# Kernel optimization log

Hardware: AMD Instinct MI355X
Metric: run time of the kernel (lower is better)

The kernel has to match this reference:

```python
import jax, jax.numpy as jnp
import numpy as np

B, T, D = 512, 128, 768
CD, SD, P = 192, 128, 128
FEAT = CD + SD + 1  # 321
LN_EPS = 1e-5


def setup_inputs() -> dict:
    key = jax.random.key(0)
    ks = jax.random.split(key, 10)
    return {
        'H': jax.random.normal(ks[0], (B, T, D), jnp.float32),
        'tt': jax.random.randint(ks[1], (B, T), 0, 2, jnp.int64),
        'attn': jnp.ones((B, T), jnp.int64),
        'Wc': jax.random.normal(ks[2], (CD, 2 * D), jnp.float32) * 0.02,
        'bc': jax.random.normal(ks[3], (CD,), jnp.float32) * 0.02,
        'Ws': jax.random.normal(ks[4], (SD, 2 * D), jnp.float32) * 0.02,
        'bs': jax.random.normal(ks[5], (SD,), jnp.float32) * 0.02,
        'gate': jnp.array([0.5], jnp.float32),
        'ln_g': jnp.ones((FEAT,), jnp.float32),
        'ln_b': jnp.zeros((FEAT,), jnp.float32),
        'Wcls': jax.random.normal(ks[6], (2, FEAT), jnp.float32) * 0.02,
        'bcls': jax.random.normal(ks[7], (2,), jnp.float32) * 0.02,
        'dirs': jax.random.normal(ks[8], (P, D), jnp.float32),
    }


def reference(H, tt, attn, Wc, bc, Ws, bs, gate, ln_g, ln_b, Wcls, bcls, dirs):
    dt = H.dtype
    cls = H[:, 0]                                   # [B, D]
    mask0 = (tt == 0) & (attn == 1)                 # [B, T]
    mask1 = (tt == 1) & (attn == 1)

    def mmean(mask):
        mf = mask.astype(dt)
        s = jnp.einsum('btd,bt->bd', H, mf)
        cnt = jnp.maximum(mask.sum(1, keepdims=True), 1).astype(dt)
        return s / cnt

    rep = jnp.concatenate([cls, mmean(mask0) - mmean(mask1)], axis=1)  # [B, 2D]
    C = rep @ Wc.T + bc
    S = rep @ Ws.T + bs
    g = jax.nn.sigmoid(gate)                        # [1]
    fused = jnp.concatenate([C * (1 - g), S * g], axis=1)  # [B, CD+SD]

    # batched max-sliced W1: project, push masked tokens to +inf, sort along T
    dirs_n = dirs / jnp.linalg.norm(dirs, axis=1, keepdims=True)
    proj = jnp.einsum('btd,pd->btp', H, dirs_n)     # [B, T, P]
    inf = jnp.asarray(jnp.inf, dt)
    xp = jnp.sort(jnp.where(mask0[:, :, None], proj, inf), axis=1)
    yp = jnp.sort(jnp.where(mask1[:, :, None], proj, inf), axis=1)
    n0 = mask0.sum(1)
    n1 = mask1.sum(1)
    mm = jnp.minimum(n0, n1)                        # [B] ragged truncation length
    valid = (jnp.arange(T)[None, :] < mm[:, None])[:, :, None]  # [B, T, 1]
    xs = jnp.where(valid, xp, 0.0)
    ys = jnp.where(valid, yp, 0.0)
    diff = jnp.abs(xs - ys).sum(1) / jnp.maximum(mm, 1)[:, None].astype(dt)  # [B, P]
    d_ot = diff.max(1, keepdims=True)               # [B, 1]

    feat = jnp.concatenate([fused, d_ot], axis=1)   # [B, 321]
    mu = feat.mean(-1, keepdims=True)
    var = feat.var(-1, keepdims=True)
    normed = (feat - mu) / jnp.sqrt(var + LN_EPS) * ln_g + ln_b
    logits = normed @ Wcls.T + bcls                 # [B, 2]

    ortho = jnp.mean((Wc @ Ws.T) ** 2)
    return logits, ortho
```

## Files before the change

kernel.cpp:

```cpp
#include <hip/hip_runtime.h>
#include <hip/hip_bf16.h>

constexpr int B_ = 512;
constexpr int T_ = 128;
constexpr int D_ = 768;
constexpr int CD_ = 192;
constexpr int SD_ = 128;
constexpr int P_ = 128;
constexpr int FEAT_ = 321;
constexpr float LN_EPS_ = 1e-5f;

constexpr size_t REP_SZ   = (size_t)B_ * 2 * D_;
constexpr size_t DN16_FLT = (size_t)P_ * D_ / 2;

typedef __attribute__((ext_vector_type(8))) short short8;
typedef __attribute__((ext_vector_type(4))) float f32x4;

__device__ __forceinline__ unsigned short f2bf(float x) {
    unsigned u = __float_as_uint(x);
    return (unsigned short)((u + 0x7FFFu + ((u >> 16) & 1u)) >> 16);
}
__device__ __forceinline__ float bf2f(unsigned short h) {
    return __uint_as_float((unsigned)h << 16);
}

__global__ __launch_bounds__(256) void k_dirs(const float* __restrict__ dirs,
                                              unsigned short* __restrict__ dn16) {
    int p = blockIdx.x;
    int tid = threadIdx.x;
    float s = 0.f;
    for (int d = tid; d < D_; d += 256) {
        float v = dirs[(size_t)p * D_ + d];
        s = fmaf(v, v, s);
    }
    __shared__ float red[256];
    red[tid] = s;
    __syncthreads();
    for (int off = 128; off > 0; off >>= 1) {
        if (tid < off) red[tid] += red[tid + off];
        __syncthreads();
    }
    float inv = 1.0f / sqrtf(red[0]);
    for (int d = tid; d < D_; d += 256) {
        dn16[(size_t)p * D_ + d] = f2bf(dirs[(size_t)p * D_ + d] * inv);
    }
}

__global__ __launch_bounds__(256) void k_rep(const float* __restrict__ H,
                                             const int* __restrict__ tt,
                                             const int* __restrict__ attn,
                                             float* __restrict__ rep) {
    int b = blockIdx.x;
    int tid = threadIdx.x;
    __shared__ float m0s[T_], m1s[T_];
    __shared__ int ncnt[2];
    if (tid < 2) ncnt[tid] = 0;
    __syncthreads();
    if (tid < T_) {
        int t = tt[b * T_ + tid];
        int a = attn[b * T_ + tid];
        float m0 = (t == 0 && a == 1) ? 1.f : 0.f;
        float m1 = (t == 1 && a == 1) ? 1.f : 0.f;
        m0s[tid] = m0;
        m1s[tid] = m1;
        if (m0 > 0.f) atomicAdd(&ncnt[0], 1);
        if (m1 > 0.f) atomicAdd(&ncnt[1], 1);
    }
    __syncthreads();
    float inv0 = 1.f / (float)max(ncnt[0], 1);
    float inv1 = 1.f / (float)max(ncnt[1], 1);
    const float* Hb = H + (size_t)b * T_ * D_;
    float* repb = rep + (size_t)b * 2 * D_;
#pragma unroll
    for (int pass = 0; pass < 3; ++pass) {
        int d = pass * 256 + tid;
        float s0 = 0.f, s1 = 0.f;
#pragma unroll 8
        for (int t = 0; t < T_; ++t) {
            float h = Hb[(size_t)t * D_ + d];
            s0 = fmaf(h, m0s[t], s0);
            s1 = fmaf(h, m1s[t], s1);
        }
        repb[d] = Hb[d];
        repb[D_ + d] = s0 * inv0 - s1 * inv1;
    }
}

constexpr int NIT_ = 24;
constexpr int BUF_U16_ = 8192;

__global__ __launch_bounds__(512, 2) void k_projsort(const float* __restrict__ H,
                                                     const int* __restrict__ tt,
                                                     const int* __restrict__ attn,
                                                     const unsigned short* __restrict__ dn16,
                                                     float* __restrict__ d_ot) {
    const int b = blockIdx.x;
    const int tid = threadIdx.x;

    __shared__ __align__(16) unsigned short stage[2 * BUF_U16_];
    __shared__ __align__(16) unsigned short proj16[T_ * 128];
    __shared__ float m0s[T_], m1s[T_];
    __shared__ unsigned char pos_s[T_];
    __shared__ int ncnt[2];
    __shared__ float dred[512];

    unsigned char* xb = (unsigned char*)stage;
    unsigned char* yb = xb + 64 * 128;

    if (tid < 2) ncnt[tid] = 0;
    __syncthreads();
    if (tid < T_) {
        int t = tt[b * T_ + tid];
        int a = attn[b * T_ + tid];
        float m0 = (t == 0 && a == 1) ? 1.f : 0.f;
        float m1 = (t == 1 && a == 1) ? 1.f : 0.f;
        m0s[tid] = m0;
        m1s[tid] = m1;
        if (m0 > 0.f) atomicAdd(&ncnt[0], 1);
        if (m1 > 0.f) atomicAdd(&ncnt[1], 1);
    }
    __syncthreads();
    const int n0 = ncnt[0], n1 = ncnt[1];
    const int ntot = n0 + n1;
    if (tid < T_) {
        float me0 = m0s[tid], me1 = m1s[tid];
        unsigned char pp = 0xFF;
        if (me0 > 0.f || me1 > 0.f) {
            bool g1 = (me1 > 0.f);
            const float* ms = g1 ? m1s : m0s;
            int pos = g1 ? n0 : 0;
            for (int j = 0; j < tid; ++j) pos += (ms[j] > 0.f) ? 1 : 0;
            pp = (unsigned char)pos;
        }
        pos_s[tid] = pp;
    }
    __syncthreads();

    const float* Hb = H + (size_t)b * T_ * D_;
    const int srow = tid >> 2;
    const int scp  = tid & 3;
    const int sclog = scp ^ ((srow >> 1) & 3);
    const float* gA = Hb + (size_t)srow * D_ + sclog * 8;
    const unsigned short* gB = dn16 + (size_t)srow * D_ + sclog * 8;
    const int dOff = srow * 32 + scp * 8;

    const int wv = tid >> 6;
    const int wr = wv >> 2;
    const int wc = wv & 3;
    const int lane = tid & 63;
    const int fr = lane & 15;
    const int kg = lane >> 4;
    const int ck = (kg ^ ((fr >> 1) & 3)) * 8;
    const int baseA = (64 * wr + fr) * 32 + ck;
    const int baseB = 4096 + (32 * wc + fr) * 32 + ck;

    f32x4 acc[4][2];
#pragma unroll
    for (int m = 0; m < 4; ++m)
#pragma unroll
        for (int n = 0; n < 2; ++n) acc[m][n] = (f32x4){0.f, 0.f, 0.f, 0.f};

    float4 a0 = *reinterpret_cast<const float4*>(gA);
    float4 a1 = *reinterpret_cast<const float4*>(gA + 4);
    short8 bv = *reinterpret_cast<const short8*>(gB);

    for (int it = 0; it < NIT_; ++it) {
        const int cur = it & 1;
        unsigned short* sb = stage + cur * BUF_U16_;
        short8 w;
        w[0] = (short)f2bf(a0.x); w[1] = (short)f2bf(a0.y);
        w[2] = (short)f2bf(a0.z); w[3] = (short)f2bf(a0.w);
        w[4] = (short)f2bf(a1.x); w[5] = (short)f2bf(a1.y);
        w[6] = (short)f2bf(a1.z); w[7] = (short)f2bf(a1.w);
        *reinterpret_cast<short8*>(sb + dOff) = w;
        *reinterpret_cast<short8*>(sb + 4096 + dOff) = bv;
        if (it < NIT_ - 1) {
            int k = (it + 1) * 32;
            a0 = *reinterpret_cast<const float4*>(gA + k);
            a1 = *reinterpret_cast<const float4*>(gA + k + 4);
            bv = *reinterpret_cast<const short8*>(gB + k);
        }
        asm volatile("s_waitcnt lgkmcnt(0)" ::: "memory");
        __builtin_amdgcn_s_barrier();
        asm volatile("" ::: "memory");

        const unsigned short* sr = stage + cur * BUF_U16_;
        short8 af[4], bf_[2];
#pragma unroll
        for (int m = 0; m < 4; ++m)
            af[m] = *reinterpret_cast<const short8*>(sr + baseA + 512 * m);
#pragma unroll
        for (int n = 0; n < 2; ++n)
            bf_[n] = *reinterpret_cast<const short8*>(sr + baseB + 512 * n);
#pragma unroll
        for (int m = 0; m < 4; ++m)
#pragma unroll
            for (int n = 0; n < 2; ++n)
                acc[m][n] = __builtin_amdgcn_mfma_f32_16x16x32_bf16(af[m], bf_[n], acc[m][n], 0, 0, 0);

        asm volatile("" ::: "memory");
        __builtin_amdgcn_s_barrier();
        asm volatile("" ::: "memory");
    }

#pragma unroll
    for (int m = 0; m < 4; ++m) {
        int row0 = 64 * wr + 16 * m + kg * 4;
#pragma unroll
        for (int r = 0; r < 4; ++r) {
            int pp = pos_s[row0 + r];
            if (pp != 0xFF) {
#pragma unroll
                for (int n = 0; n < 2; ++n) {
                    int col = 32 * wc + 16 * n + fr;
                    unsigned bb = f2bf(acc[m][n][r]);
                    unsigned su = bb ^ ((bb >> 15) ? 0xFFFFu : 0x8000u);
                    proj16[pp * 128 + col] = (unsigned short)su;
                }
            }
        }
    }
    __syncthreads();

    const int mmv = min(n0, n1);
    const int c = tid & 127;
    const int q = tid >> 7;
#pragma unroll
    for (int pass = 0; pass < 2; ++pass) {
        const int pbase = q * 32 + pass * 16;
        unsigned kv[16];
        int cnt[16];
#pragma unroll
        for (int ii = 0; ii < 16; ++ii) {
            int p = pbase + ii;
            unsigned key = 0xFFFFFFFFu;
            if (p < ntot) {
                unsigned su = proj16[p * 128 + c];
                key = ((unsigned)(p >= n0) << 31) | (su << 8) | (unsigned)p;
            }
            kv[ii] = key;
            cnt[ii] = 0;
        }
        int lo, hi;
        if (pbase + 16 <= n0) { lo = 0;  hi = n0;   }
        else if (pbase >= n0) { lo = n0; hi = ntot; }
        else                  { lo = 0;  hi = ntot; }
        for (int j = lo; j < hi; ++j) {
            unsigned su = proj16[j * 128 + c];
            unsigned kw = ((unsigned)(j >= n0) << 31) | (su << 8) | (unsigned)j;
#pragma unroll
            for (int ii = 0; ii < 16; ++ii) cnt[ii] += (kw < kv[ii]) ? 1 : 0;
        }
#pragma unroll
        for (int ii = 0; ii < 16; ++ii) {
            int p = pbase + ii;
            if (p < ntot) {
                int rank = cnt[ii] - ((p >= n0 && lo == 0) ? n0 : 0);
                if (rank < mmv) {
                    unsigned char* buf = (p >= n0) ? yb : xb;
                    buf[rank * 128 + c] = (unsigned char)p;
                }
            }
        }
    }
    __syncthreads();

    float part = 0.f;
    for (int r = q; r < mmv; r += 4) {
        unsigned sx = proj16[(int)xb[r * 128 + c] * 128 + c];
        unsigned sy = proj16[(int)yb[r * 128 + c] * 128 + c];
        unsigned bx = sx ^ ((sx >> 15) ? 0x8000u : 0xFFFFu);
        unsigned by = sy ^ ((sy >> 15) ? 0x8000u : 0xFFFFu);
        part += fabsf(bf2f((unsigned short)bx) - bf2f((unsigned short)by));
    }
    dred[tid] = part;
    __syncthreads();
    if (tid < 128) {
        float invm = 1.f / (float)max(mmv, 1);
        dred[tid] = (dred[tid] + dred[tid + 128] + dred[tid + 256] + dred[tid + 384]) * invm;
    }
    __syncthreads();
    if (tid < 64) {
        float m = fmaxf(dred[tid], dred[tid + 64]);
#pragma unroll
        for (int off = 32; off > 0; off >>= 1) m = fmaxf(m, __shfl_xor(m, off));
        if (tid == 0) d_ot[b] = m;
    }
}

__global__ __launch_bounds__(320) void k_head(const float* __restrict__ rep,
                                              const float* __restrict__ Wc,
                                              const float* __restrict__ bc,
                                              const float* __restrict__ Ws,
                                              const float* __restrict__ bs,
                                              const float* __restrict__ gate,
                                              const float* __restrict__ lng,
                                              const float* __restrict__ lnb,
                                              const float* __restrict__ Wcls,
                                              const float* __restrict__ bcls,
                                              const float* __restrict__ d_ot,
                                              float* __restrict__ out) {
    int b0 = blockIdx.x * 4;
    int tid = threadIdx.x;
    __shared__ __align__(16) float repS[4 * 1536];
    __shared__ float featS[4 * FEAT_];

    const float4* repg = reinterpret_cast<const float4*>(rep + (size_t)b0 * 1536);
    float4* repl = reinterpret_cast<float4*>(repS);
    for (int i = tid; i < 1536; i += 320) repl[i] = repg[i];
    __syncthreads();

    float g = 1.f / (1.f + expf(-gate[0]));

    {
        int o = tid;
        bool isC = o < CD_;
        const float* w = isC ? (Wc + (size_t)o * 1536) : (Ws + (size_t)(o - CD_) * 1536);
        float bias = isC ? bc[o] : bs[o - CD_];
        float scale = isC ? (1.f - g) : g;
        const float4* w4 = reinterpret_cast<const float4*>(w);
        float a0 = 0.f, a1 = 0.f, a2 = 0.f, a3 = 0.f;
        for (int k4 = 0; k4 < 384; ++k4) {
            float4 wv = w4[k4];
            float4 r0 = repl[k4];
            float4 r1 = repl[384 + k4];
            float4 r2 = repl[768 + k4];
            float4 r3 = repl[1152 + k4];
            a0 += fmaf(wv.x, r0.x, fmaf(wv.y, r0.y, fmaf(wv.z, r0.z, wv.w * r0.w)));
            a1 += fmaf(wv.x, r1.x, fmaf(wv.y, r1.y, fmaf(wv.z, r1.z, wv.w * r1.w)));
            a2 += fmaf(wv.x, r2.x, fmaf(wv.y, r2.y, fmaf(wv.z, r2.z, wv.w * r2.w)));
            a3 += fmaf(wv.x, r3.x, fmaf(wv.y, r3.y, fmaf(wv.z, r3.z, wv.w * r3.w)));
        }
        featS[0 * FEAT_ + o] = (a0 + bias) * scale;
        featS[1 * FEAT_ + o] = (a1 + bias) * scale;
        featS[2 * FEAT_ + o] = (a2 + bias) * scale;
        featS[3 * FEAT_ + o] = (a3 + bias) * scale;
    }
    if (tid < 4) featS[tid * FEAT_ + 320] = d_ot[b0 + tid];
    __syncthreads();

    int w = tid >> 6, lane = tid & 63;
    if (w < 4) {
        const float* f = featS + w * FEAT_;
        float s = 0.f, s2 = 0.f;
        for (int i = lane; i < FEAT_; i += 64) {
            float v = f[i];
            s += v;
            s2 = fmaf(v, v, s2);
        }
#pragma unroll
        for (int off = 32; off > 0; off >>= 1) {
            s += __shfl_xor(s, off);
            s2 += __shfl_xor(s2, off);
        }
        float mu = s * (1.f / (float)FEAT_);
        float var = fmaxf(s2 * (1.f / (float)FEAT_) - mu * mu, 0.f);
        float rstd = 1.0f / sqrtf(var + LN_EPS_);
        float l0 = 0.f, l1 = 0.f;
        for (int i = lane; i < FEAT_; i += 64) {
            float nv = (f[i] - mu) * rstd * lng[i] + lnb[i];
            l0 = fmaf(nv, Wcls[i], l0);
            l1 = fmaf(nv, Wcls[FEAT_ + i], l1);
        }
#pragma unroll
        for (int off = 32; off > 0; off >>= 1) {
            l0 += __shfl_xor(l0, off);
            l1 += __shfl_xor(l1, off);
        }
        if (lane == 0) {
            out[(size_t)(b0 + w) * 2 + 0] = l0 + bcls[0];
            out[(size_t)(b0 + w) * 2 + 1] = l1 + bcls[1];
        }
    }
}

__global__ __launch_bounds__(256) void k_ortho(const float* __restrict__ Wc,
                                               const float* __restrict__ Ws,
                                               float* __restrict__ part) {
    int i = blockIdx.x;
    int tid = threadIdx.x;
    __shared__ float wrow[1536];
    __shared__ float tmp[256];
    for (int k = tid; k < 1536; k += 256) wrow[k] = Wc[(size_t)i * 1536 + k];
    __syncthreads();
    int j = tid & 127, h = tid >> 7;
    const float* wsr = Ws + (size_t)j * 1536 + h * 768;
    const float* wr = wrow + h * 768;
    float s = 0.f;
    for (int k = 0; k < 768; ++k) s = fmaf(wr[k], wsr[k], s);
    tmp[tid] = s;
    __syncthreads();
    if (tid < 128) {
        float d = tmp[tid] + tmp[tid + 128];
        tmp[tid] = d * d;
    }
    __syncthreads();
    for (int off = 64; off > 0; off >>= 1) {
        if (tid < off) tmp[tid] += tmp[tid + off];
        __syncthreads();
    }
    if (tid == 0) part[i] = tmp[0];
}

__global__ __launch_bounds__(256) void k_ortho2(const float* __restrict__ part,
                                                float* __restrict__ out) {
    int tid = threadIdx.x;
    __shared__ float red[256];
    red[tid] = (tid < CD_) ? part[tid] : 0.f;
    __syncthreads();
    for (int off = 128; off > 0; off >>= 1) {
        if (tid < off) red[tid] += red[tid + off];
        __syncthreads();
    }
    if (tid == 0) out[(size_t)B_ * 2] = red[0] / (float)(CD_ * SD_);
}

extern "C" void kernel_launch(void* const* d_in, const int* in_sizes, int n_in,
                              void* d_out, int out_size, void* d_ws, size_t ws_size,
                              hipStream_t stream) {
    const float* H    = (const float*)d_in[0];
    const int*   tt   = (const int*)d_in[1];
    const int*   attn = (const int*)d_in[2];
    const float* Wc   = (const float*)d_in[3];
    const float* bc   = (const float*)d_in[4];
    const float* Ws   = (const float*)d_in[5];
    const float* bs   = (const float*)d_in[6];
    const float* gate = (const float*)d_in[7];
    const float* lng  = (const float*)d_in[8];
    const float* lnb  = (const float*)d_in[9];
    const float* Wcls = (const float*)d_in[10];
    const float* bcls = (const float*)d_in[11];
    const float* dirs = (const float*)d_in[12];

    float* ws    = (float*)d_ws;
    float* rep   = ws;
    unsigned short* dn16 = (unsigned short*)(ws + REP_SZ);
    float* dot   = ws + REP_SZ + DN16_FLT;
    float* part  = dot + B_;
    float* out   = (float*)d_out;

    k_dirs<<<P_, 256, 0, stream>>>(dirs, dn16);
    k_rep<<<B_, 256, 0, stream>>>(H, tt, attn, rep);
    k_projsort<<<B_, 512, 0, stream>>>(H, tt, attn, dn16, dot);
    k_head<<<B_ / 4, 320, 0, stream>>>(rep, Wc, bc, Ws, bs, gate, lng, lnb, Wcls, bcls, dot, out);
    k_ortho<<<CD_, 256, 0, stream>>>(Wc, Ws, part);
    k_ortho2<<<1, 256, 0, stream>>>(part, out);
}
```

Baseline: 218.7 us.

## Fuse masked-mean rep computation into projection kernel using MFMA on staged H

Removes the separate k_rep kernel and computes the masked token means inside k_projsort. It reuses each bf16 H tile already staged for the projection GEMM, transposing it into shared memory and reducing it with an extra MFMA against bf16 mask vectors on two waves. The CLS row is written straight from the fp32 prefetch registers. The global prefetch is also deepened to two stages by unrolling the K loop in pairs. This avoids a second full read of H from HBM, at the cost of more LDS and extra work inside the loop, and the means are now computed from bf16-rounded H.

```diff
diff --git a/kernel.cpp b/kernel.cpp
--- a/kernel.cpp
+++ b/kernel.cpp
@@ -46,14 +46,46 @@
     }
 }
 
-__global__ __launch_bounds__(256) void k_rep(const float* __restrict__ H,
-                                             const int* __restrict__ tt,
-                                             const int* __restrict__ attn,
-                                             float* __restrict__ rep) {
-    int b = blockIdx.x;
-    int tid = threadIdx.x;
+constexpr int NIT_ = 24;
+constexpr int BUF_U16_ = 8192;
+constexpr int HT_STR_ = 136;
+
+__global__ __launch_bounds__(512, 2) void k_projsort(const float* __restrict__ H,
+                                                     const int* __restrict__ tt,
+                                                     const int* __restrict__ attn,
+                                                     const unsigned short* __restrict__ dn16,
+                                                     float* __restrict__ rep,
+                                                     float* __restrict__ d_ot) {
+    const int b = blockIdx.x;
+    const int tid = threadIdx.x;
+
+    __shared__ __align__(16) unsigned short stage[2 * BUF_U16_];
+    __shared__ __align__(16) unsigned short Ht[32 * HT_STR_];
+    __shared__ __align__(16) unsigned short proj16[T_ * 128];
+    __shared__ __align__(16) unsigned short mask16[2 * T_];
     __shared__ float m0s[T_], m1s[T_];
+    __shared__ unsigned char pos_s[T_];
     __shared__ int ncnt[2];
+    __shared__ float dred[512];
+
+    unsigned char* xb = (unsigned char*)stage;
+    unsigned char* yb = xb + 64 * 128;
+
+    const float* Hb = H + (size_t)b * T_ * D_;
+    const int srow = tid >> 2;
+    const int scp  = tid & 3;
+    const int sclog = scp ^ ((srow >> 1) & 3);
+    const float* gA = Hb + (size_t)srow * D_ + sclog * 8;
+    const unsigned short* gB = dn16 + (size_t)srow * D_ + sclog * 8;
+    const int dOff = srow * 32 + scp * 8;
+
+    float4 a0A = *reinterpret_cast<const float4*>(gA);
+    float4 a1A = *reinterpret_cast<const float4*>(gA + 4);
+    short8 bvA = *reinterpret_cast<const short8*>(gB);
+    float4 a0B = *reinterpret_cast<const float4*>(gA + 32);
+    float4 a1B = *reinterpret_cast<const float4*>(gA + 36);
+    short8 bvB = *reinterpret_cast<const short8*>(gB + 32);
+
     if (tid < 2) ncnt[tid] = 0;
     __syncthreads();
     if (tid < T_) {
@@ -63,65 +95,16 @@
         float m1 = (t == 1 && a == 1) ? 1.f : 0.f;
         m0s[tid] = m0;
         m1s[tid] = m1;
+        mask16[tid] = (m0 > 0.f) ? 0x3F80u : 0u;
+        mask16[T_ + tid] = (m1 > 0.f) ? 0x3F80u : 0u;
         if (m0 > 0.f) atomicAdd(&ncnt[0], 1);
         if (m1 > 0.f) atomicAdd(&ncnt[1], 1);
     }
     __syncthreads();
-    float inv0 = 1.f / (float)max(ncnt[0], 1);
-    float inv1 = 1.f / (float)max(ncnt[1], 1);
-    const float* Hb = H + (size_t)b * T_ * D_;
-    float* repb = rep + (size_t)b * 2 * D_;
-#pragma unroll
-    for (int pass = 0; pass < 3; ++pass) {
-        int d = pass * 256 + tid;
-        float s0 = 0.f, s1 = 0.f;
-#pragma unroll 8
-        for (int t = 0; t < T_; ++t) {
-            float h = Hb[(size_t)t * D_ + d];
-            s0 = fmaf(h, m0s[t], s0);
-            s1 = fmaf(h, m1s[t], s1);
-        }
-        repb[d] = Hb[d];
-        repb[D_ + d] = s0 * inv0 - s1 * inv1;
-    }
-}
-
-constexpr int NIT_ = 24;
-constexpr int BUF_U16_ = 8192;
-
-__global__ __launch_bounds__(512, 2) void k_projsort(const float* __restrict__ H,
-                                                     const int* __restrict__ tt,
-                                                     const int* __restrict__ attn,
-                                                     const unsigned short* __restrict__ dn16,
-                                                     float* __restrict__ d_ot) {
-    const int b = blockIdx.x;
-    const int tid = threadIdx.x;
-
-    __shared__ __align__(16) unsigned short stage[2 * BUF_U16_];
-    __shared__ __align__(16) unsigned short proj16[T_ * 128];
-    __shared__ float m0s[T_], m1s[T_];
-    __shared__ unsigned char pos_s[T_];
-    __shared__ int ncnt[2];
-    __shared__ float dred[512];
-
-    unsigned char* xb = (unsigned char*)stage;
-    unsigned char* yb = xb + 64 * 128;
-
-    if (tid < 2) ncnt[tid] = 0;
-    __syncthreads();
-    if (tid < T_) {
-        int t = tt[b * T_ + tid];
-        int a = attn[b * T_ + tid];
-        float m0 = (t == 0 && a == 1) ? 1.f : 0.f;
-        float m1 = (t == 1 && a == 1) ? 1.f : 0.f;
-        m0s[tid] = m0;
-        m1s[tid] = m1;
-        if (m0 > 0.f) atomicAdd(&ncnt[0], 1);
-        if (m1 > 0.f) atomicAdd(&ncnt[1], 1);
-    }
-    __syncthreads();
     const int n0 = ncnt[0], n1 = ncnt[1];
     const int ntot = n0 + n1;
+    const float inv0 = 1.f / (float)max(n0, 1);
+    const float inv1 = 1.f / (float)max(n1, 1);
     if (tid < T_) {
         float me0 = m0s[tid], me1 = m1s[tid];
         unsigned char pp = 0xFF;
@@ -136,23 +119,19 @@
     }
     __syncthreads();
 
-    const float* Hb = H + (size_t)b * T_ * D_;
-    const int srow = tid >> 2;
-    const int scp  = tid & 3;
-    const int sclog = scp ^ ((srow >> 1) & 3);
-    const float* gA = Hb + (size_t)srow * D_ + sclog * 8;
-    const unsigned short* gB = dn16 + (size_t)srow * D_ + sclog * 8;
-    const int dOff = srow * 32 + scp * 8;
-
     const int wv = tid >> 6;
     const int wr = wv >> 2;
     const int wc = wv & 3;
     const int lane = tid & 63;
     const int fr = lane & 15;
     const int kg = lane >> 4;
+    const int fk = kg * 8;
     const int ck = (kg ^ ((fr >> 1) & 3)) * 8;
     const int baseA = (64 * wr + fr) * 32 + ck;
-    const int baseB = 4096 + (32 * wc + fr) * 32 + ck;
+    const int baseB = 4096 + (32 * wc + 16 * 0 + fr) * 32 + ck;
+    const bool repw = (wv >= 6);
+    const int jf = wv & 1;
+    float* repb = rep + (size_t)b * 2 * D_;
 
     f32x4 acc[4][2];
 #pragma unroll
@@ -160,47 +139,62 @@
 #pragma unroll
         for (int n = 0; n < 2; ++n) acc[m][n] = (f32x4){0.f, 0.f, 0.f, 0.f};
 
-    float4 a0 = *reinterpret_cast<const float4*>(gA);
-    float4 a1 = *reinterpret_cast<const float4*>(gA + 4);
-    short8 bv = *reinterpret_cast<const short8*>(gB);
-
-    for (int it = 0; it < NIT_; ++it) {
-        const int cur = it & 1;
-        unsigned short* sb = stage + cur * BUF_U16_;
+    auto body = [&](int it, unsigned short* sb, float4& pa0, float4& pa1, short8& pbv) {
         short8 w;
-        w[0] = (short)f2bf(a0.x); w[1] = (short)f2bf(a0.y);
-        w[2] = (short)f2bf(a0.z); w[3] = (short)f2bf(a0.w);
-        w[4] = (short)f2bf(a1.x); w[5] = (short)f2bf(a1.y);
-        w[6] = (short)f2bf(a1.z); w[7] = (short)f2bf(a1.w);
+        w[0] = (short)f2bf(pa0.x); w[1] = (short)f2bf(pa0.y);
+        w[2] = (short)f2bf(pa0.z); w[3] = (short)f2bf(pa0.w);
+        w[4] = (short)f2bf(pa1.x); w[5] = (short)f2bf(pa1.y);
+        w[6] = (short)f2bf(pa1.z); w[7] = (short)f2bf(pa1.w);
         *reinterpret_cast<short8*>(sb + dOff) = w;
-        *reinterpret_cast<short8*>(sb + 4096 + dOff) = bv;
-        if (it < NIT_ - 1) {
-            int k = (it + 1) * 32;
-            a0 = *reinterpret_cast<const float4*>(gA + k);
-            a1 = *reinterpret_cast<const float4*>(gA + k + 4);
-            bv = *reinterpret_cast<const short8*>(gB + k);
+        *reinterpret_cast<short8*>(sb + 4096 + dOff) = pbv;
+#pragma unroll
+        for (int j = 0; j < 8; ++j)
+            Ht[(sclog * 8 + j) * HT_STR_ + srow] = (unsigned short)w[j];
+        if (srow == 0) {
+            *reinterpret_cast<float4*>(repb + it * 32 + sclog * 8) = pa0;
+            *reinterpret_cast<float4*>(repb + it * 32 + sclog * 8 + 4) = pa1;
+        }
+        if (it + 2 < NIT_) {
+            pa0 = *reinterpret_cast<const float4*>(gA + (it + 2) * 32);
+            pa1 = *reinterpret_cast<const float4*>(gA + (it + 2) * 32 + 4);
+            pbv = *reinterpret_cast<const short8*>(gB + (it + 2) * 32);
         }
         asm volatile("s_waitcnt lgkmcnt(0)" ::: "memory");
         __builtin_amdgcn_s_barrier();
         asm volatile("" ::: "memory");
 
-        const unsigned short* sr = stage + cur * BUF_U16_;
         short8 af[4], bf_[2];
 #pragma unroll
         for (int m = 0; m < 4; ++m)
-            af[m] = *reinterpret_cast<const short8*>(sr + baseA + 512 * m);
+            af[m] = *reinterpret_cast<const short8*>(sb + baseA + 512 * m);
 #pragma unroll
         for (int n = 0; n < 2; ++n)
-            bf_[n] = *reinterpret_cast<const short8*>(sr + baseB + 512 * n);
+            bf_[n] = *reinterpret_cast<const short8*>(sb + baseB + 512 * n);
 #pragma unroll
         for (int m = 0; m < 4; ++m)
 #pragma unroll
             for (int n = 0; n < 2; ++n)
                 acc[m][n] = __builtin_amdgcn_mfma_f32_16x16x32_bf16(af[m], bf_[n], acc[m][n], 0, 0, 0);
 
+        if (repw) {
+            f32x4 ar = (f32x4){0.f, 0.f, 0.f, 0.f};
+#pragma unroll
+            for (int tc = 0; tc < 4; ++tc) {
+                short8 am = {0, 0, 0, 0, 0, 0, 0, 0};
+                if (fr < 2) am = *reinterpret_cast<const short8*>(&mask16[fr * T_ + tc * 32 + fk]);
+                short8 bm = *reinterpret_cast<const short8*>(&Ht[(16 * jf + fr) * HT_STR_ + tc * 32 + fk]);
+                ar = __builtin_amdgcn_mfma_f32_16x16x32_bf16(am, bm, ar, 0, 0, 0);
+            }
+            if (lane < 16) repb[D_ + it * 32 + jf * 16 + lane] = ar[0] * inv0 - ar[1] * inv1;
+        }
         asm volatile("" ::: "memory");
         __builtin_amdgcn_s_barrier();
         asm volatile("" ::: "memory");
+    };
+
+    for (int i2 = 0; i2 < NIT_ / 2; ++i2) {
+        body(2 * i2,     stage,            a0A, a1A, bvA);
+        body(2 * i2 + 1, stage + BUF_U16_, a0B, a1B, bvB);
     }
 
 #pragma unroll
@@ -440,8 +434,7 @@
     float* out   = (float*)d_out;
 
     k_dirs<<<P_, 256, 0, stream>>>(dirs, dn16);
-    k_rep<<<B_, 256, 0, stream>>>(H, tt, attn, rep);
-    k_projsort<<<B_, 512, 0, stream>>>(H, tt, attn, dn16, dot);
+    k_projsort<<<B_, 512, 0, stream>>>(H, tt, attn, dn16, rep, dot);
     k_head<<<B_ / 4, 320, 0, stream>>>(rep, Wc, bc, Ws, bs, gate, lng, lnb, Wcls, bcls, dot, out);
     k_ortho<<<CD_, 256, 0, stream>>>(Wc, Ws, part);
     k_ortho2<<<1, 256, 0, stream>>>(part, out);
```

Result: faster. 191.3 us (-12.5%).
